# Kernel optimization log

Measured on AMD Instinct MI355X. Metric: run time of the kernel, lower is better.

Reference implementation:

```python
import jax, jax.numpy as jnp
import numpy as np

KS = 25      # kernel_size (odd)
STRIDE = 2


def _parabolic_kernel(t, ks):
    # torch: linspace(-ks//2 + 1, ks//2, ks); for odd ks this is -half..half
    half = ks // 2
    z = jnp.linspace(-half, half, ks, dtype=jnp.float32)
    return -(z ** 2)[None, :] / (4.0 * t[:, None])  # (C, ks)


def setup_inputs() -> dict:
    key = jax.random.key(0)
    kf, kt = jax.random.split(key)
    f = jax.random.normal(kf, (16, 128, 16384), dtype=jnp.float32)
    # learned per-channel scale, init uniform(0, 4) as in the torch module
    t = jax.random.uniform(kt, (128,), dtype=jnp.float32, minval=0.0, maxval=4.0)
    return {"f": f, "t": t}


def reference(f, t):
    # Banded max-plus parabolic dilation: out[b,c,i] = max_d f[b,c,i+d-half] + h[c,d]
    # (the original materializes CxNxN banded matrices; this is the O(N*ks) form)
    B, C, N = f.shape
    h = _parabolic_kernel(t, KS)                      # (C, KS)
    half = KS // 2
    pad = jnp.pad(f, ((0, 0), (0, 0), (half, half)), constant_values=-jnp.inf)
    out = jnp.full_like(f, -jnp.inf)
    for d in range(KS):                               # fixed small kernel loop
        out = jnp.maximum(out, pad[:, :, d:d + N] + h[:, d][None, :, None])
    # stride subsampling along the spatial dim
    return out[:, :, ::STRIDE]
```

## Files before the change

### kernel.cpp

```cpp
#include <hip/hip_runtime.h>
#include <cmath>

#define KS     25
#define HALF   12
#define N_IN   16384
#define N_OUT  8192
#define C_DIM  128
#define B_DIM  16

#define OPT    8
#define TPB    256
#define OUT_PER_BLOCK (OPT * TPB)
#define SEGS   (N_OUT / OUT_PER_BLOCK)
#define NV     (2 * OPT + KS - 1 + 1)

__global__ __launch_bounds__(TPB) void parabolic_pool_kernel(
    const float* __restrict__ f,
    const float* __restrict__ t,
    float* __restrict__ out) {

  const int blk = blockIdx.x;
  const int seg = blk & (SEGS - 1);
  const int row = blk >> 2;
  const int c   = row & (C_DIM - 1);

  const float* __restrict__ frow = f + (size_t)row * N_IN;
  float* __restrict__ orow       = out + (size_t)row * N_OUT;

  const float tc   = t[c];
  const float minv = -0.25f / tc;
  float h[KS];
#pragma unroll
  for (int d = 0; d < KS; ++d) {
    const float z = (float)(d - HALF);
    h[d] = (z * z) * minv;
  }

  const int o_t   = seg * OUT_PER_BLOCK + (int)threadIdx.x * OPT;
  const int jbase = 2 * o_t - HALF;

  float v[NV];
  if (jbase >= 0 && jbase + NV <= N_IN) {
#pragma unroll
    for (int q = 0; q < NV / 4; ++q) {
      const float4 x = *reinterpret_cast<const float4*>(frow + jbase + 4 * q);
      v[4 * q + 0] = x.x;
      v[4 * q + 1] = x.y;
      v[4 * q + 2] = x.z;
      v[4 * q + 3] = x.w;
    }
  } else {
#pragma unroll
    for (int k = 0; k < NV; ++k) {
      const int j = jbase + k;
      v[k] = (j >= 0 && j < N_IN) ? frow[j] : -INFINITY;
    }
  }

  float acc[OPT];
#pragma unroll
  for (int o = 0; o < OPT; ++o) {
    float m = v[2 * o] + h[0];
#pragma unroll
    for (int d = 1; d < KS; ++d) {
      m = fmaxf(m, v[2 * o + d] + h[d]);
    }
    acc[o] = m;
  }

  *reinterpret_cast<float4*>(orow + o_t) =
      make_float4(acc[0], acc[1], acc[2], acc[3]);
  *reinterpret_cast<float4*>(orow + o_t + 4) =
      make_float4(acc[4], acc[5], acc[6], acc[7]);
}

extern "C" void kernel_launch(void* const* d_in, const int* in_sizes, int n_in,
                              void* d_out, int out_size, void* d_ws, size_t ws_size,
                              hipStream_t stream) {
  const float* f = (const float*)d_in[0];
  const float* t = (const float*)d_in[1];
  float* out     = (float*)d_out;

  const int grid = B_DIM * C_DIM * SEGS;
  parabolic_pool_kernel<<<grid, TPB, 0, stream>>>(f, t, out);
}
```

Measured before the change: 36.63 us.

## Stage input window in padded LDS to remove overlapping global halo loads

Each block now loads its whole input window (4128 floats) cooperatively into shared memory with coalesced vector loads. One float of padding per 16 reduces bank conflicts. Threads then read their 40-element windows from LDS instead of each issuing overlapping global float4 loads covering about 2.5x its own span. This cuts redundant global and L2 traffic at the cost of a block-wide barrier and about 17 KB of LDS per block, which may limit occupancy.

```diff
diff --git a/kernel.cpp b/kernel.cpp
--- a/kernel.cpp
+++ b/kernel.cpp
@@ -10,25 +10,54 @@
 
 #define OPT    8
 #define TPB    256
-#define OUT_PER_BLOCK (OPT * TPB)
-#define SEGS   (N_OUT / OUT_PER_BLOCK)
-#define NV     (2 * OPT + KS - 1 + 1)
+#define OUT_BLK (OPT * TPB)
+#define SEGS   (N_OUT / OUT_BLK)
+#define NF     4128
+#define NGRAN  (NF / 4)
+#define LDS_F  (NF + NF / 16)
+
+typedef float f32x4 __attribute__((ext_vector_type(4)));
 
 __global__ __launch_bounds__(TPB) void parabolic_pool_kernel(
     const float* __restrict__ f,
     const float* __restrict__ t,
     float* __restrict__ out) {
 
+  __shared__ float lds[LDS_F];
+
   const int blk = blockIdx.x;
   const int seg = blk & (SEGS - 1);
   const int row = blk >> 2;
   const int c   = row & (C_DIM - 1);
+  const int tid = threadIdx.x;
 
   const float* __restrict__ frow = f + (size_t)row * N_IN;
   float* __restrict__ orow       = out + (size_t)row * N_OUT;
 
-  const float tc   = t[c];
-  const float minv = -0.25f / tc;
+  const int o0    = seg * OUT_BLK;
+  const int gbase = 2 * o0 - HALF;
+
+#pragma unroll
+  for (int i = 0; i < (NGRAN + TPB - 1) / TPB; ++i) {
+    const int g = i * TPB + tid;
+    if (g < NGRAN) {
+      const int j  = 4 * g;
+      const int p  = j + (g >> 2);
+      const int gf = gbase + j;
+      if (gf >= 0 && gf + 4 <= N_IN) {
+        *reinterpret_cast<f32x4*>(&lds[p]) =
+            *reinterpret_cast<const f32x4*>(frow + gf);
+      } else {
+#pragma unroll
+        for (int k = 0; k < 4; ++k) {
+          const int jj = gf + k;
+          lds[p + k] = (jj >= 0 && jj < N_IN) ? frow[jj] : -INFINITY;
+        }
+      }
+    }
+  }
+
+  const float minv = -0.25f / t[c];
   float h[KS];
 #pragma unroll
   for (int d = 0; d < KS; ++d) {
@@ -36,42 +65,49 @@
     h[d] = (z * z) * minv;
   }
 
-  const int o_t   = seg * OUT_PER_BLOCK + (int)threadIdx.x * OPT;
-  const int jbase = 2 * o_t - HALF;
+  __syncthreads();
 
-  float v[NV];
-  if (jbase >= 0 && jbase + NV <= N_IN) {
+  float w[40];
 #pragma unroll
-    for (int q = 0; q < NV / 4; ++q) {
-      const float4 x = *reinterpret_cast<const float4*>(frow + jbase + 4 * q);
-      v[4 * q + 0] = x.x;
-      v[4 * q + 1] = x.y;
-      v[4 * q + 2] = x.z;
-      v[4 * q + 3] = x.w;
+  for (int m = 0; m < 2; ++m) {
+    const int p = 17 * (tid + m);
+#pragma unroll
+    for (int q = 0; q < 4; ++q) {
+      const f32x4 x = *reinterpret_cast<const f32x4*>(&lds[p + 4 * q]);
+      w[16 * m + 4 * q + 0] = x.x;
+      w[16 * m + 4 * q + 1] = x.y;
+      w[16 * m + 4 * q + 2] = x.z;
+      w[16 * m + 4 * q + 3] = x.w;
     }
-  } else {
+  }
+  {
+    const int p = 17 * (tid + 2);
 #pragma unroll
-    for (int k = 0; k < NV; ++k) {
-      const int j = jbase + k;
-      v[k] = (j >= 0 && j < N_IN) ? frow[j] : -INFINITY;
+    for (int q = 0; q < 2; ++q) {
+      const f32x4 x = *reinterpret_cast<const f32x4*>(&lds[p + 4 * q]);
+      w[32 + 4 * q + 0] = x.x;
+      w[32 + 4 * q + 1] = x.y;
+      w[32 + 4 * q + 2] = x.z;
+      w[32 + 4 * q + 3] = x.w;
     }
   }
 
   float acc[OPT];
 #pragma unroll
   for (int o = 0; o < OPT; ++o) {
-    float m = v[2 * o] + h[0];
+    float m = w[2 * o] + h[0];
 #pragma unroll
     for (int d = 1; d < KS; ++d) {
-      m = fmaxf(m, v[2 * o + d] + h[d]);
+      m = fmaxf(m, w[2 * o + d] + h[d]);
     }
     acc[o] = m;
   }
 
-  *reinterpret_cast<float4*>(orow + o_t) =
-      make_float4(acc[0], acc[1], acc[2], acc[3]);
-  *reinterpret_cast<float4*>(orow + o_t + 4) =
-      make_float4(acc[4], acc[5], acc[6], acc[7]);
+  const int o_t = o0 + tid * OPT;
+  *reinterpret_cast<f32x4*>(orow + o_t) =
+      (f32x4){acc[0], acc[1], acc[2], acc[3]};
+  *reinterpret_cast<f32x4*>(orow + o_t + 4) =
+      (f32x4){acc[4], acc[5], acc[6], acc[7]};
 }
 
 extern "C" void kernel_launch(void* const* d_in, const int* in_sizes, int n_in,
```

After: 39.09 us. 6.7% more time.
